# Kernel optimization log

Hardware: AMD Instinct MI355X
Metric: run time of the kernel (lower is better)

## Reference

```python
import jax, jax.numpy as jnp
import numpy as np

D_MODEL = 512
N_HEADS = 8
BLOCK = 512
D_HEAD = D_MODEL // N_HEADS
SCALE = D_HEAD ** -0.5


def _linear_params(key, d_in, d_out):
    kw, kb = jax.random.split(key)
    bound = 1.0 / np.sqrt(d_in)
    w = jax.random.uniform(kw, (d_in, d_out), jnp.float32, -bound, bound)
    b = jax.random.uniform(kb, (d_out,), jnp.float32, -bound, bound)
    return w, b


def setup_inputs() -> dict:
    key = jax.random.key(0)
    keys = jax.random.split(key, 10)
    x = jax.random.normal(keys[0], (4, 8192, D_MODEL), jnp.float32)
    names = ["lq", "lk", "lv", "lo", "gq", "gk", "gv", "go"]
    inp = {"x": x}
    for i, n in enumerate(names):
        w, b = _linear_params(keys[1 + i], D_MODEL, D_MODEL)
        inp[n + "_w"] = w
        inp[n + "_b"] = b
    gw, gb = _linear_params(keys[9], 2 * D_MODEL, D_MODEL)
    inp["gate_w"] = gw
    inp["gate_b"] = gb
    return inp


def _attend(q, k, v):
    # q,k,v: (..., L, H, Dh) -> (..., L, H, Dh)
    scores = jnp.einsum("...qhd,...khd->...hqk", q, k) * SCALE
    probs = jax.nn.softmax(scores, axis=-1)
    return jnp.einsum("...hqk,...khd->...qhd", probs, v)


def reference(x, lq_w, lq_b, lk_w, lk_b, lv_w, lv_b, lo_w, lo_b,
              gq_w, gq_b, gk_w, gk_b, gv_w, gv_b, go_w, go_b,
              gate_w, gate_b):
    B, S, D = x.shape
    nb = S // BLOCK
    xb = x.reshape(B, nb, BLOCK, D)

    def heads(t, L_axes):
        return t.reshape(t.shape[:-1] + (N_HEADS, D_HEAD))

    # block-local attention (all blocks batched)
    Q = heads(xb @ lq_w + lq_b, None)  # (B, nb, bs, H, Dh)
    K = heads(xb @ lk_w + lk_b, None)
    V = heads(xb @ lv_w + lv_b, None)
    loc = _attend(Q, K, V).reshape(B, nb, BLOCK, D)
    local_out = (loc @ lo_w + lo_b).reshape(B, S, D)

    # pooled block summaries: AdaptiveAvgPool1d(1) == mean over block length
    pooled = xb.mean(axis=2)  # (B, nb, D)
    Qg = heads(pooled @ gq_w + gq_b, None)  # (B, nb, H, Dh)
    Kg = heads(pooled @ gk_w + gk_b, None)
    Vg = heads(pooled @ gv_w + gv_b, None)
    glob = _attend(Qg, Kg, Vg).reshape(B, nb, D)
    glob = glob @ go_w + go_b  # (B, nb, D)

    # broadcast each block summary to its tokens
    global_out = jnp.repeat(glob, BLOCK, axis=1)  # (B, S, D)

    gate_in = jnp.concatenate([local_out, global_out], axis=-1)
    gate = jax.nn.sigmoid(gate_in @ gate_w + gate_b)
    return gate * local_out + (1.0 - gate) * global_out
```

## Files before the change

### kernel.cpp

```cpp
#include <hip/hip_runtime.h>
#include <math.h>

typedef unsigned short u16;
typedef short s16;
typedef u16 u16x8 __attribute__((ext_vector_type(8)));
typedef u16 u16x4 __attribute__((ext_vector_type(4)));
typedef s16 s16x8 __attribute__((ext_vector_type(8)));
typedef float f32x4 __attribute__((ext_vector_type(4)));
typedef unsigned u32x4 __attribute__((ext_vector_type(4)));

__device__ __forceinline__ float b2f(u16 u) { return __uint_as_float(((unsigned)u) << 16); }
__device__ __forceinline__ u16 f2b(float f) {
  unsigned x = __float_as_uint(f);
  unsigned r = x + 0x7fffu + ((x >> 16) & 1u);
  return (u16)(r >> 16);
}
__device__ __forceinline__ unsigned cvtpk(float a, float b) {
  unsigned r;
  asm("v_cvt_pk_bf16_f32 %0, %1, %2" : "=v"(r) : "v"(a), "v"(b));
  return r;
}
union PkH { u32x4 w; s16x8 h; };
union Pk2 { unsigned w[2]; u16x4 h; };

#define SCALE 0.125f
#define SCLG2E 0.1803368801111137f
#define DM 512
#define NTOK 32768

typedef __attribute__((address_space(1))) unsigned int as1_u32;
typedef __attribute__((address_space(3))) unsigned int as3_u32;
__device__ __forceinline__ void gl2lds16(const u16* g, u16* s) {
  __builtin_amdgcn_global_load_lds((as1_u32*)g, (as3_u32*)s, 16, 0, 0);
}

__global__ __launch_bounds__(256)
void conv_psum(const float* __restrict__ X, u16* __restrict__ Xb,
               float* __restrict__ Psum)
{
  __shared__ float ps[4][512];
  const int tid = threadIdx.x;
  const int c8 = (tid & 63) * 8;
  const int rg = tid >> 6;
  const size_t tok0 = (size_t)blockIdx.x * 64;
  f32x4 s0 = {0.f, 0.f, 0.f, 0.f}, s1 = {0.f, 0.f, 0.f, 0.f};
  for (int it = 0; it < 16; ++it) {
    const size_t tok = tok0 + it * 4 + rg;
    const float* xp = X + tok * DM + c8;
    f32x4 a = *(const f32x4*)xp;
    f32x4 b = *(const f32x4*)(xp + 4);
    Pk2 p0, p1;
    p0.w[0] = cvtpk(a[0], a[1]); p0.w[1] = cvtpk(a[2], a[3]);
    p1.w[0] = cvtpk(b[0], b[1]); p1.w[1] = cvtpk(b[2], b[3]);
    *(u16x4*)(Xb + tok * DM + c8)     = p0.h;
    *(u16x4*)(Xb + tok * DM + c8 + 4) = p1.h;
    s0 += a; s1 += b;
  }
  *(f32x4*)&ps[rg][c8]     = s0;
  *(f32x4*)&ps[rg][c8 + 4] = s1;
  __syncthreads();
#pragma unroll
  for (int i = 0; i < 2; ++i) {
    const int col = tid + i * 256;
    Psum[(size_t)blockIdx.x * DM + col] =
        ps[0][col] + ps[1][col] + ps[2][col] + ps[3][col];
  }
}

__global__ __launch_bounds__(256)
void pool_prep(const float* __restrict__ Psum, u16* __restrict__ PB)
{
  const int g = blockIdx.x, tid = threadIdx.x;
#pragma unroll
  for (int i = 0; i < 2; ++i) {
    const int col = tid + i * 256;
    float v = 0.f;
#pragma unroll
    for (int s = 0; s < 8; ++s) v += Psum[(size_t)(g * 8 + s) * DM + col];
    PB[(size_t)g * DM + col] = f2b(v * (1.f / 512.f));
  }
}

__global__ __launch_bounds__(256)
void trans_w(const float* w0, const float* w1, const float* w2, const float* w3,
             const float* w4, const float* w5, const float* w6, const float* w7,
             const float* w8, const float* w9, u16* __restrict__ WT)
{
  __shared__ float t[32][33];
  const int z = blockIdx.z;
  const float* W = (z == 0) ? w0 : (z == 1) ? w1 : (z == 2) ? w2 : (z == 3) ? w3 :
                   (z == 4) ? w4 : (z == 5) ? w5 : (z == 6) ? w6 : (z == 7) ? w7 :
                   (z == 8) ? w8 : w9;
  u16* D = WT + (size_t)z * DM * DM;
  const int tx = threadIdx.x & 31, ty = threadIdx.x >> 5;
  const int n0 = blockIdx.x * 32, k0 = blockIdx.y * 32;
#pragma unroll
  for (int j = 0; j < 4; ++j)
    t[ty + j * 8][tx] = W[(size_t)(k0 + ty + j * 8) * DM + n0 + tx];
  __syncthreads();
#pragma unroll
  for (int j = 0; j < 4; ++j)
    D[(size_t)(n0 + ty + j * 8) * DM + k0 + tx] = f2b(t[tx][ty + j * 8]);
}

__global__ __launch_bounds__(256)
void conv_w(const float* __restrict__ W, u16* __restrict__ D)
{
  const size_t i = ((size_t)blockIdx.x * 256 + threadIdx.x) * 8;
  f32x4 a = *(const f32x4*)(W + i);
  f32x4 b = *(const f32x4*)(W + i + 4);
  Pk2 p0, p1;
  p0.w[0] = cvtpk(a[0], a[1]); p0.w[1] = cvtpk(a[2], a[3]);
  p1.w[0] = cvtpk(b[0], b[1]); p1.w[1] = cvtpk(b[2], b[3]);
  *(u16x4*)(D + i)     = p0.h;
  *(u16x4*)(D + i + 4) = p1.h;
}

__global__ __launch_bounds__(256)
void bc_kernel(const float* __restrict__ go_b, const float* __restrict__ gate_w,
               const float* __restrict__ gate_b, float* __restrict__ bc)
{
  __shared__ float red[8][32];
  const int tid = threadIdx.x;
  const int jj = tid & 31, part = tid >> 5;
  const int j = blockIdx.x * 32 + jj;
  float p = 0.f;
#pragma unroll
  for (int i = 0; i < 64; ++i) {
    const int k = part * 64 + i;
    p = fmaf(go_b[k], gate_w[(size_t)(512 + k) * DM + j], p);
  }
  red[part][jj] = p;
  __syncthreads();
  if (tid < 32) {
    float v = gate_b[blockIdx.x * 32 + tid];
#pragma unroll
    for (int s = 0; s < 8; ++s) v += red[s][tid];
    bc[blockIdx.x * 32 + tid] = v;
  }
}

template<int EPI>
__global__ __launch_bounds__(256)
void gemm_mfma(const u16* __restrict__ A, const u16* __restrict__ Wt,
               const float* __restrict__ bias, u16* __restrict__ Cb,
               float* __restrict__ Cf, float outscale,
               const float* __restrict__ GG)
{
  __shared__ u16 As[2][128 * 64];
  __shared__ u16 Bs[2][128 * 64];
  const int tid = threadIdx.x;
  const int w = tid >> 6, l = tid & 63;
  const int l15 = l & 15, gl = l >> 4;
  const int wm = w >> 1, wn = w & 1;

  int mt, nt;
  if (gridDim.y == 256) {
    const int H = blockIdx.y * 4 + blockIdx.x;
    const int xcd = H & 7, i = H >> 3;
    mt = xcd * 32 + (i >> 2);
    nt = i & 3;
  } else {
    mt = blockIdx.y; nt = blockIdx.x;
  }
  const int m0 = mt * 128, n0 = nt * 128;

  const int srow = l >> 3;
  const int scol = ((l & 7) ^ (srow & 7)) * 8;
  const u16* Ag = A  + (size_t)(m0 + w * 32 + srow) * DM + scol;
  const u16* Bg = Wt + (size_t)(n0 + w * 32 + srow) * DM + scol;

  auto stage = [&](int t, int b) {
    const int k0 = t * 64;
#pragma unroll
    for (int c = 0; c < 4; ++c) {
      gl2lds16(Ag + (size_t)(c * 8) * DM + k0, &As[b][(w * 32 + c * 8) * 64]);
      gl2lds16(Bg + (size_t)(c * 8) * DM + k0, &Bs[b][(w * 32 + c * 8) * 64]);
    }
  };

  f32x4 acc[4][4];
#pragma unroll
  for (int i = 0; i < 4; ++i)
#pragma unroll
    for (int j = 0; j < 4; ++j) acc[i][j] = {0.f, 0.f, 0.f, 0.f};

  const int xorv = l15 & 7;
  stage(0, 0);
#pragma unroll
  for (int t = 0; t < 8; ++t) {
    if (t < 7) {
      stage(t + 1, (t + 1) & 1);
      asm volatile("s_waitcnt vmcnt(8)" ::: "memory");
    } else {
      asm volatile("s_waitcnt vmcnt(0)" ::: "memory");
    }
    __builtin_amdgcn_s_barrier();
    __builtin_amdgcn_sched_barrier(0);
    const int b = t & 1;
#pragma unroll
    for (int kd = 0; kd < 2; ++kd) {
      const int go = ((gl + 4 * kd) ^ xorv) * 8;
      s16x8 af[4], bfr[4];
#pragma unroll
      for (int f = 0; f < 4; ++f) {
        af[f]  = *(const s16x8*)&As[b][(wm * 64 + f * 16 + l15) * 64 + go];
        bfr[f] = *(const s16x8*)&Bs[b][(wn * 64 + f * 16 + l15) * 64 + go];
      }
#pragma unroll
      for (int fm = 0; fm < 4; ++fm)
#pragma unroll
        for (int fn = 0; fn < 4; ++fn) {
          if (EPI == 2)
            acc[fm][fn] = __builtin_amdgcn_mfma_f32_16x16x32_bf16(
                af[fm], bfr[fn], acc[fm][fn], 0, 0, 0);
          else
            acc[fm][fn] = __builtin_amdgcn_mfma_f32_16x16x32_bf16(
                bfr[fn], af[fm], acc[fm][fn], 0, 0, 0);
        }
    }
    __builtin_amdgcn_s_barrier();
  }

  if (EPI == 2) {
#pragma unroll
    for (int fn = 0; fn < 4; ++fn) {
      const int n = n0 + wn * 64 + fn * 16 + l15;
      const float bn = bias[n];
      const int d = n & 63, ghn = n >> 6;
#pragma unroll
      for (int fm = 0; fm < 4; ++fm) {
        const int m = m0 + wm * 64 + fm * 16 + gl * 4;
        const int f = (m & 63) >> 4;
        const int pos = ((f >> 1) << 5) | (gl << 3) | ((f & 1) << 2);
        Pk2 p;
        p.w[0] = cvtpk(acc[fm][fn][0] + bn, acc[fm][fn][1] + bn);
        p.w[1] = cvtpk(acc[fm][fn][2] + bn, acc[fm][fn][3] + bn);
        *(u16x4*)(Cb + ((size_t)(((m >> 9) * 8 + ghn) * 64 + d)) * 512
                     + ((m & 511) >> 6) * 64 + pos) = p.h;
      }
    }
  } else {
#pragma unroll
    for (int fm = 0; fm < 4; ++fm) {
      const int m = m0 + wm * 64 + fm * 16 + l15;
      const int brow = m >> 9;
#pragma unroll
      for (int fn = 0; fn < 4; ++fn) {
        const int nb = n0 + wn * 64 + fn * 16 + gl * 4;
        if (EPI == 0) {
          f32x4 b4 = *(const f32x4*)&bias[nb];
          f32x4 v = (acc[fm][fn] + b4) * outscale;
          Pk2 p;
          p.w[0] = cvtpk(v[0], v[1]);
          p.w[1] = cvtpk(v[2], v[3]);
          *(u16x4*)(Cb + (size_t)m * DM + nb) = p.h;
        } else if (EPI == 3) {
          Pk2 p;
          p.w[0] = cvtpk(acc[fm][fn][0], acc[fm][fn][1]);
          p.w[1] = cvtpk(acc[fm][fn][2], acc[fm][fn][3]);
          *(u16x4*)(Cb + (size_t)m * DM + nb) = p.h;
        } else {
          f32x4 z = acc[fm][fn] + *(const f32x4*)&GG[(size_t)brow * 1024 + 512 + nb];
          u16x4 lo4 = *(const u16x4*)(A + (size_t)m * DM + nb);
          f32x4 go4 = *(const f32x4*)&GG[(size_t)brow * 1024 + nb];
          f32x4 res;
#pragma unroll
          for (int r = 0; r < 4; ++r) {
            float g = 1.f / (1.f + __expf(-z[r]));
            res[r] = g * b2f(lo4[r]) + (1.f - g) * go4[r];
          }
          *(f32x4*)(Cf + (size_t)m * DM + nb) = res;
        }
      }
    }
  }
}

__global__ __launch_bounds__(256)
void gemm64(const u16* __restrict__ A,
            const u16* B0, const u16* B1, const u16* B2,
            const float* b0, const float* b1, const float* b2,
            float* __restrict__ Out, int ldo)
{
  __shared__ u16 As[2][64 * 64];
  __shared__ u16 Bs[2][128 * 64];
  const int tid = threadIdx.x;
  const int w = tid >> 6, l = tid & 63;
  const int l15 = l & 15, gl = l >> 4;
  const int bx = blockIdx.x;
  const int grp = bx >> 2;
  const u16* Bt = ((grp == 0) ? B0 : (grp == 1) ? B1 : B2)
                  + (size_t)(bx & 3) * 128 * DM;
  const float* bias = (grp == 0) ? b0 : (grp == 1) ? b1 : b2;

  const int srow = l >> 3;
  const int scol = ((l & 7) ^ (srow & 7)) * 8;
  const u16* Ag = A  + (size_t)(w * 16 + srow) * DM + scol;
  const u16* Bg = Bt + (size_t)(w * 32 + srow) * DM + scol;

  auto stage = [&](int t, int b) {
    const int k0 = t * 64;
#pragma unroll
    for (int c = 0; c < 2; ++c)
      gl2lds16(Ag + (size_t)(c * 8) * DM + k0, &As[b][(w * 16 + c * 8) * 64]);
#pragma unroll
    for (int c = 0; c < 4; ++c)
      gl2lds16(Bg + (size_t)(c * 8) * DM + k0, &Bs[b][(w * 32 + c * 8) * 64]);
  };

  f32x4 acc[4][2];
#pragma unroll
  for (int i = 0; i < 4; ++i)
#pragma unroll
    for (int j = 0; j < 2; ++j) acc[i][j] = {0.f, 0.f, 0.f, 0.f};

  const int xorv = l15 & 7;
  stage(0, 0);
#pragma unroll
  for (int t = 0; t < 8; ++t) {
    if (t < 7) {
      stage(t + 1, (t + 1) & 1);
      asm volatile("s_waitcnt vmcnt(6)" ::: "memory");
    } else {
      asm volatile("s_waitcnt vmcnt(0)" ::: "memory");
    }
    __builtin_amdgcn_s_barrier();
    __builtin_amdgcn_sched_barrier(0);
    const int b = t & 1;
#pragma unroll
    for (int kd = 0; kd < 2; ++kd) {
      const int go = ((gl + 4 * kd) ^ xorv) * 8;
      s16x8 af[4], bfr[2];
#pragma unroll
      for (int f = 0; f < 4; ++f)
        af[f] = *(const s16x8*)&As[b][(f * 16 + l15) * 64 + go];
#pragma unroll
      for (int f = 0; f < 2; ++f)
        bfr[f] = *(const s16x8*)&Bs[b][(w * 32 + f * 16 + l15) * 64 + go];
#pragma unroll
      for (int fm = 0; fm < 4; ++fm)
#pragma unroll
        for (int fn = 0; fn < 2; ++fn)
          acc[fm][fn] = __builtin_amdgcn_mfma_f32_16x16x32_bf16(
              bfr[fn], af[fm], acc[fm][fn], 0, 0, 0);
    }
    __builtin_amdgcn_s_barrier();
  }

#pragma unroll
  for (int fm = 0; fm < 4; ++fm) {
    const int m = fm * 16 + l15;
#pragma unroll
    for (int fn = 0; fn < 2; ++fn) {
      const int nloc = w * 32 + fn * 16 + gl * 4;
      f32x4 b4 = *(const f32x4*)&bias[(bx & 3) * 128 + nloc];
      *(f32x4*)&Out[(size_t)m * ldo + bx * 128 + nloc] = acc[fm][fn] + b4;
    }
  }
}

__global__ __launch_bounds__(512, 4)
void attn_mfma(const u16* __restrict__ Q, const u16* __restrict__ K,
               const u16* __restrict__ VT, u16* __restrict__ CTX)
{
  __shared__ u16 Ks[64 * 64];
  __shared__ u16 VsT[64 * 64];
  const int tid = threadIdx.x;
  const int w = tid >> 6, l = tid & 63;
  const int l15 = l & 15, gl = l >> 4;
  const int g = blockIdx.x, h = blockIdx.y, qh = blockIdx.z;
  const int t0 = g * 512;
  const int fb = h * 64;
  const int q0 = t0 + qh * 256 + w * 32;
  const u16* VTb = VT + ((size_t)(g * 8 + h) * 64) * 512;

  s16x8 qf[2][2];
#pragma unroll
  for (int fq = 0; fq < 2; ++fq)
#pragma unroll
    for (int kd = 0; kd < 2; ++kd)
      qf[fq][kd] = *(const s16x8*)(Q + (size_t)(q0 + fq * 16 + l15) * DM
                                     + fb + gl * 8 + kd * 32);

  f32x4 o[2][4];
#pragma unroll
  for (int i = 0; i < 2; ++i)
#pragma unroll
    for (int j = 0; j < 4; ++j) o[i][j] = {0.f, 0.f, 0.f, 0.f};
  f32x4 psv[2] = {{0.f,0.f,0.f,0.f}, {0.f,0.f,0.f,0.f}};

  const int srow = tid >> 3;
  const int swg = ((tid & 7) ^ ((tid >> 3) & 7)) * 8;
  const u16* Kg = K + (size_t)(t0 + srow) * DM + fb + swg;
  const u16* Vg = VTb + (size_t)srow * 512 + swg;
  s16x8 kreg = *(const s16x8*)Kg;
  s16x8 vreg = *(const s16x8*)Vg;
  const int sw = l15 & 7;

  for (int kc = 0; kc < 8; ++kc) {
    __syncthreads();
    *(s16x8*)&Ks[tid * 8]  = kreg;
    *(s16x8*)&VsT[tid * 8] = vreg;
    __syncthreads();
    if (kc < 7) {
      kreg = *(const s16x8*)(Kg + (size_t)(kc + 1) * 64 * DM);
      vreg = *(const s16x8*)(Vg + (kc + 1) * 64);
    }

    f32x4 s[4][2];
#pragma unroll
    for (int i = 0; i < 4; ++i)
#pragma unroll
      for (int j = 0; j < 2; ++j) s[i][j] = {0.f, 0.f, 0.f, 0.f};
#pragma unroll
    for (int kd = 0; kd < 2; ++kd) {
      s16x8 kf[4];
#pragma unroll
      for (int fm = 0; fm < 4; ++fm)
        kf[fm] = *(const s16x8*)&Ks[(fm * 16 + l15) * 64 + ((gl + 4 * kd) ^ sw) * 8];
#pragma unroll
      for (int fm = 0; fm < 4; ++fm)
#pragma unroll
        for (int fq = 0; fq < 2; ++fq)
          s[fm][fq] = __builtin_amdgcn_mfma_f32_16x16x32_bf16(
              kf[fm], qf[fq][kd], s[fm][fq], 0, 0, 0);
    }

#pragma unroll
    for (int fq = 0; fq < 2; ++fq)
#pragma unroll
      for (int fm = 0; fm < 4; ++fm) {
#pragma unroll
        for (int r = 0; r < 4; ++r) s[fm][fq][r] = exp2f(s[fm][fq][r]);
        psv[fq] += s[fm][fq];
      }

    PkH pf[2][2];
#pragma unroll
    for (int ka = 0; ka < 2; ++ka)
#pragma unroll
      for (int fq = 0; fq < 2; ++fq) {
        pf[ka][fq].w[0] = cvtpk(s[2 * ka][fq][0], s[2 * ka][fq][1]);
        pf[ka][fq].w[1] = cvtpk(s[2 * ka][fq][2], s[2 * ka][fq][3]);
        pf[ka][fq].w[2] = cvtpk(s[2 * ka + 1][fq][0], s[2 * ka + 1][fq][1]);
        pf[ka][fq].w[3] = cvtpk(s[2 * ka + 1][fq][2], s[2 * ka + 1][fq][3]);
      }

#pragma unroll
    for (int ka = 0; ka < 2; ++ka)
#pragma unroll
      for (int fd = 0; fd < 4; ++fd) {
        s16x8 vf = *(const s16x8*)&VsT[(fd * 16 + l15) * 64 + ((ka * 4 + gl) ^ sw) * 8];
#pragma unroll
        for (int qm = 0; qm < 2; ++qm)
          o[qm][fd] = __builtin_amdgcn_mfma_f32_16x16x32_bf16(
              pf[ka][qm].h, vf, o[qm][fd], 0, 0, 0);
      }
  }

  float l_[2];
#pragma unroll
  for (int fq = 0; fq < 2; ++fq) {
    float t = (psv[fq][0] + psv[fq][1]) + (psv[fq][2] + psv[fq][3]);
    t += __shfl_xor(t, 16);
    t += __shfl_xor(t, 32);
    l_[fq] = t;
  }
#pragma unroll
  for (int qm = 0; qm < 2; ++qm) {
    const float i0 = 1.f / __shfl(l_[qm], gl * 4 + 0);
    const float i1 = 1.f / __shfl(l_[qm], gl * 4 + 1);
    const float i2 = 1.f / __shfl(l_[qm], gl * 4 + 2);
    const float i3 = 1.f / __shfl(l_[qm], gl * 4 + 3);
#pragma unroll
    for (int fd = 0; fd < 4; ++fd) {
      const size_t base = (size_t)(q0 + qm * 16 + gl * 4) * DM + fb + fd * 16 + l15;
      CTX[base]          = f2b(o[qm][fd][0] * i0);
      CTX[base + DM]     = f2b(o[qm][fd][1] * i1);
      CTX[base + 2 * DM] = f2b(o[qm][fd][2] * i2);
      CTX[base + 3 * DM] = f2b(o[qm][fd][3] * i3);
    }
  }
}

__global__ __launch_bounds__(256)
void gattn(const float* __restrict__ QKVg, u16* __restrict__ GlB)
{
  __shared__ float q[16][64], k[16][64], v[16][64];
  __shared__ float sc[16][16];
  const int bh = blockIdx.x;
  const int b = bh >> 3, h = bh & 7;
  const int tid = threadIdx.x;
  for (int idx = tid; idx < 1024; idx += 256) {
    const int n = idx >> 6, d = idx & 63;
    const size_t off = (size_t)(b * 16 + n) * 1536 + h * 64 + d;
    q[n][d] = QKVg[off]; k[n][d] = QKVg[off + 512]; v[n][d] = QKVg[off + 1024];
  }
  __syncthreads();
  {
    const int qq = tid >> 4, kk = tid & 15;
    float s = 0.f;
#pragma unroll
    for (int d = 0; d < 64; ++d) s = fmaf(q[qq][d], k[kk][d], s);
    sc[qq][kk] = s * SCALE;
  }
  __syncthreads();
  if (tid < 16) {
    float mx = -INFINITY;
#pragma unroll
    for (int j = 0; j < 16; ++j) mx = fmaxf(mx, sc[tid][j]);
    float e[16]; float sum = 0.f;
#pragma unroll
    for (int j = 0; j < 16; ++j) { e[j] = __expf(sc[tid][j] - mx); sum += e[j]; }
    const float inv = 1.f / sum;
#pragma unroll
    for (int j = 0; j < 16; ++j) sc[tid][j] = e[j] * inv;
  }
  __syncthreads();
  for (int idx = tid; idx < 1024; idx += 256) {
    const int qq = idx >> 6, d = idx & 63;
    float o = 0.f;
#pragma unroll
    for (int j = 0; j < 16; ++j) o = fmaf(sc[qq][j], v[j][d], o);
    GlB[(size_t)(b * 16 + qq) * DM + h * 64 + d] = f2b(o);
  }
}

extern "C" void kernel_launch(void* const* d_in, const int* in_sizes, int n_in,
                              void* d_out, int out_size, void* d_ws, size_t ws_size,
                              hipStream_t stream)
{
  const float* x      = (const float*)d_in[0];
  const float* lq_w   = (const float*)d_in[1];
  const float* lq_b   = (const float*)d_in[2];
  const float* lk_w   = (const float*)d_in[3];
  const float* lk_b   = (const float*)d_in[4];
  const float* lv_w   = (const float*)d_in[5];
  const float* lv_b   = (const float*)d_in[6];
  const float* lo_w   = (const float*)d_in[7];
  const float* lo_b   = (const float*)d_in[8];
  const float* gq_w   = (const float*)d_in[9];
  const float* gq_b   = (const float*)d_in[10];
  const float* gk_w   = (const float*)d_in[11];
  const float* gk_b   = (const float*)d_in[12];
  const float* gv_w   = (const float*)d_in[13];
  const float* gv_b   = (const float*)d_in[14];
  const float* go_w   = (const float*)d_in[15];
  const float* go_b   = (const float*)d_in[16];
  const float* gate_w = (const float*)d_in[17];
  const float* gate_b = (const float*)d_in[18];
  float* out = (float*)d_out;

  const size_t NE = (size_t)NTOK * DM;
  const size_t DD = (size_t)DM * DM;
  char* ws = (char*)d_ws;
  u16* Qb  = (u16*)ws;
  u16* Kb  = Qb + NE;
  u16* VT  = Kb + NE;
  u16* WT  = VT + NE;
  u16* goD = WT + 10 * DD;
  u16* WcT = goD + DD;
  u16* PB  = WcT + DD;
  u16* GlB = PB + 64 * DM;
  float* scr  = (float*)(GlB + 64 * DM);
  float* Psum = scr;
  float* QKVg = Psum + 512 * DM;
  float* GG   = QKVg + (size_t)64 * 1536;
  float* bc   = GG + (size_t)64 * 1024;
  u16* xb = (u16*)d_out;
  u16* LOCAL = Kb;

  u16* WTq  = WT;
  u16* WTk  = WT + 1 * DD;
  u16* WTv  = WT + 2 * DD;
  u16* WTo  = WT + 3 * DD;
  u16* WTg  = WT + 4 * DD;
  u16* WTgq = WT + 5 * DD;
  u16* WTgk = WT + 6 * DD;
  u16* WTgv = WT + 7 * DD;
  u16* WTgo = WT + 8 * DD;
  u16* WTg2 = WT + 9 * DD;

  conv_psum<<<512, 256, 0, stream>>>(x, xb, Psum);
  trans_w<<<dim3(16, 16, 10), 256, 0, stream>>>(
      lq_w, lk_w, lv_w, lo_w, gate_w, gq_w, gk_w, gv_w, go_w,
      gate_w + DD, WT);
  conv_w<<<128, 256, 0, stream>>>(go_w, goD);
  bc_kernel<<<16, 256, 0, stream>>>(go_b, gate_w, gate_b, bc);
  pool_prep<<<64, 256, 0, stream>>>(Psum, PB);

  const dim3 gg(4, 256), bb(256);
  gemm_mfma<0><<<gg, bb, 0, stream>>>(xb, WTq, lq_b, Qb, nullptr, SCLG2E, nullptr);
  gemm_mfma<0><<<gg, bb, 0, stream>>>(xb, WTk, lk_b, Kb, nullptr, 1.0f, nullptr);
  gemm_mfma<2><<<gg, bb, 0, stream>>>(xb, WTv, lv_b, VT, nullptr, 1.0f, nullptr);
  gemm_mfma<3><<<dim3(4, 4), bb, 0, stream>>>(WTg2, goD, nullptr, WcT, nullptr, 1.0f, nullptr);

  attn_mfma<<<dim3(64, 8, 2), 512, 0, stream>>>(Qb, Kb, VT, Qb );
  gemm_mfma<0><<<gg, bb, 0, stream>>>(Qb , WTo, lo_b, LOCAL, nullptr, 1.0f, nullptr);

  gemm64<<<12, 256, 0, stream>>>(PB, WTgq, WTgk, WTgv, gq_b, gk_b, gv_b, QKVg, 1536);
  gattn<<<32, 256, 0, stream>>>(QKVg, GlB);
  gemm64<<<8, 256, 0, stream>>>(GlB, WTgo, WcT, WcT, go_b, bc, bc, GG, 1024);

  gemm_mfma<1><<<gg, bb, 0, stream>>>(LOCAL, WTg, nullptr, nullptr, out, 1.0f, GG);
}
```

Before: 243.1 us.

## Fuse Q/K/V projection GEMMs into one launch and compute softmax row sums via MFMA

Replaces three separate Q, K and V projection GEMM launches with one kernel over a 12x256 grid, where each tile picks its weight, bias and epilogue from its N-tile index. This cuts launch overhead and lets all three projections share one wave schedule with better occupancy. In the attention kernel, the per-lane exp-sum accumulation and cross-lane shuffle reduction are replaced by an extra MFMA against a vector of bf16 ones, so the normalisers come out in the accumulator layout. That sum now uses the bf16-rounded probabilities, matching the P·V numerator, at the cost of a few more MFMA issues.

```diff
diff --git a/kernel.cpp b/kernel.cpp
--- a/kernel.cpp
+++ b/kernel.cpp
@@ -140,6 +140,131 @@
   }
 }
 
+__global__ __launch_bounds__(256)
+void gemm_qkv(const u16* __restrict__ A,
+              const u16* __restrict__ WTq, const u16* __restrict__ WTk,
+              const u16* __restrict__ WTv,
+              const float* __restrict__ bq, const float* __restrict__ bk,
+              const float* __restrict__ bv,
+              u16* __restrict__ Qb, u16* __restrict__ Kb, u16* __restrict__ VT)
+{
+  __shared__ u16 As[2][128 * 64];
+  __shared__ u16 Bs[2][128 * 64];
+  const int tid = threadIdx.x;
+  const int w = tid >> 6, l = tid & 63;
+  const int l15 = l & 15, gl = l >> 4;
+  const int wm = w >> 1, wn = w & 1;
+
+  const int H = blockIdx.y * 12 + blockIdx.x;
+  const int xcd = H & 7, i = H >> 3;
+  const int mt = xcd * 32 + i / 12;
+  const int nt = i % 12;
+  const int sel = nt >> 2;
+  const int m0 = mt * 128;
+  const int n0 = (nt & 3) * 128;
+
+  const u16* Wt = (sel == 0) ? WTq : (sel == 1) ? WTk : WTv;
+  const float* bias = (sel == 0) ? bq : (sel == 1) ? bk : bv;
+
+  const int srow = l >> 3;
+  const int scol = ((l & 7) ^ (srow & 7)) * 8;
+  const u16* Ag = A  + (size_t)(m0 + w * 32 + srow) * DM + scol;
+  const u16* Bg = Wt + (size_t)(n0 + w * 32 + srow) * DM + scol;
+
+  auto stage = [&](int t, int b) {
+    const int k0 = t * 64;
+#pragma unroll
+    for (int c = 0; c < 4; ++c) {
+      gl2lds16(Ag + (size_t)(c * 8) * DM + k0, &As[b][(w * 32 + c * 8) * 64]);
+      gl2lds16(Bg + (size_t)(c * 8) * DM + k0, &Bs[b][(w * 32 + c * 8) * 64]);
+    }
+  };
+
+  f32x4 acc[4][4];
+#pragma unroll
+  for (int ii = 0; ii < 4; ++ii)
+#pragma unroll
+    for (int j = 0; j < 4; ++j) acc[ii][j] = {0.f, 0.f, 0.f, 0.f};
+
+  const int xorv = l15 & 7;
+  stage(0, 0);
+#pragma unroll
+  for (int t = 0; t < 8; ++t) {
+    if (t < 7) {
+      stage(t + 1, (t + 1) & 1);
+      asm volatile("s_waitcnt vmcnt(8)" ::: "memory");
+    } else {
+      asm volatile("s_waitcnt vmcnt(0)" ::: "memory");
+    }
+    __builtin_amdgcn_s_barrier();
+    __builtin_amdgcn_sched_barrier(0);
+    const int b = t & 1;
+#pragma unroll
+    for (int kd = 0; kd < 2; ++kd) {
+      const int go = ((gl + 4 * kd) ^ xorv) * 8;
+      s16x8 af[4], bfr[4];
+#pragma unroll
+      for (int f = 0; f < 4; ++f) {
+        af[f]  = *(const s16x8*)&As[b][(wm * 64 + f * 16 + l15) * 64 + go];
+        bfr[f] = *(const s16x8*)&Bs[b][(wn * 64 + f * 16 + l15) * 64 + go];
+      }
+      if (sel == 2) {
+#pragma unroll
+        for (int fm = 0; fm < 4; ++fm)
+#pragma unroll
+          for (int fn = 0; fn < 4; ++fn)
+            acc[fm][fn] = __builtin_amdgcn_mfma_f32_16x16x32_bf16(
+                af[fm], bfr[fn], acc[fm][fn], 0, 0, 0);
+      } else {
+#pragma unroll
+        for (int fm = 0; fm < 4; ++fm)
+#pragma unroll
+          for (int fn = 0; fn < 4; ++fn)
+            acc[fm][fn] = __builtin_amdgcn_mfma_f32_16x16x32_bf16(
+                bfr[fn], af[fm], acc[fm][fn], 0, 0, 0);
+      }
+    }
+    __builtin_amdgcn_s_barrier();
+  }
+
+  if (sel == 2) {
+#pragma unroll
+    for (int fn = 0; fn < 4; ++fn) {
+      const int n = n0 + wn * 64 + fn * 16 + l15;
+      const float bn = bias[n];
+      const int d = n & 63, ghn = n >> 6;
+#pragma unroll
+      for (int fm = 0; fm < 4; ++fm) {
+        const int m = m0 + wm * 64 + fm * 16 + gl * 4;
+        const int f = (m & 63) >> 4;
+        const int pos = ((f >> 1) << 5) | (gl << 3) | ((f & 1) << 2);
+        Pk2 p;
+        p.w[0] = cvtpk(acc[fm][fn][0] + bn, acc[fm][fn][1] + bn);
+        p.w[1] = cvtpk(acc[fm][fn][2] + bn, acc[fm][fn][3] + bn);
+        *(u16x4*)(VT + ((size_t)(((m >> 9) * 8 + ghn) * 64 + d)) * 512
+                     + ((m & 511) >> 6) * 64 + pos) = p.h;
+      }
+    }
+  } else {
+    u16* Cb = (sel == 0) ? Qb : Kb;
+    const float sc = (sel == 0) ? SCLG2E : 1.0f;
+#pragma unroll
+    for (int fm = 0; fm < 4; ++fm) {
+      const int m = m0 + wm * 64 + fm * 16 + l15;
+#pragma unroll
+      for (int fn = 0; fn < 4; ++fn) {
+        const int nb = n0 + wn * 64 + fn * 16 + gl * 4;
+        f32x4 b4 = *(const f32x4*)&bias[nb];
+        f32x4 v = (acc[fm][fn] + b4) * sc;
+        Pk2 p;
+        p.w[0] = cvtpk(v[0], v[1]);
+        p.w[1] = cvtpk(v[2], v[3]);
+        *(u16x4*)(Cb + (size_t)m * DM + nb) = p.h;
+      }
+    }
+  }
+}
+
 template<int EPI>
 __global__ __launch_bounds__(256)
 void gemm_mfma(const u16* __restrict__ A, const u16* __restrict__ Wt,
@@ -210,68 +335,43 @@
 #pragma unroll
       for (int fm = 0; fm < 4; ++fm)
 #pragma unroll
-        for (int fn = 0; fn < 4; ++fn) {
-          if (EPI == 2)
-            acc[fm][fn] = __builtin_amdgcn_mfma_f32_16x16x32_bf16(
-                af[fm], bfr[fn], acc[fm][fn], 0, 0, 0);
-          else
-            acc[fm][fn] = __builtin_amdgcn_mfma_f32_16x16x32_bf16(
-                bfr[fn], af[fm], acc[fm][fn], 0, 0, 0);
+        for (int fn = 0; fn < 4; ++fn)
+          acc[fm][fn] = __builtin_amdgcn_mfma_f32_16x16x32_bf16(
+              bfr[fn], af[fm], acc[fm][fn], 0, 0, 0);
+    }
+    __builtin_amdgcn_s_barrier();
+  }
+
+#pragma unroll
+  for (int fm = 0; fm < 4; ++fm) {
+    const int m = m0 + wm * 64 + fm * 16 + l15;
+    const int brow = m >> 9;
+#pragma unroll
+    for (int fn = 0; fn < 4; ++fn) {
+      const int nb = n0 + wn * 64 + fn * 16 + gl * 4;
+      if (EPI == 0) {
+        f32x4 b4 = *(const f32x4*)&bias[nb];
+        f32x4 v = (acc[fm][fn] + b4) * outscale;
+        Pk2 p;
+        p.w[0] = cvtpk(v[0], v[1]);
+        p.w[1] = cvtpk(v[2], v[3]);
+        *(u16x4*)(Cb + (size_t)m * DM + nb) = p.h;
+      } else if (EPI == 3) {
+        Pk2 p;
+        p.w[0] = cvtpk(acc[fm][fn][0], acc[fm][fn][1]);
+        p.w[1] = cvtpk(acc[fm][fn][2], acc[fm][fn][3]);
+        *(u16x4*)(Cb + (size_t)m * DM + nb) = p.h;
+      } else {
+        f32x4 z = acc[fm][fn] + *(const f32x4*)&GG[(size_t)brow * 1024 + 512 + nb];
+        u16x4 lo4 = *(const u16x4*)(A + (size_t)m * DM + nb);
+        f32x4 go4 = *(const f32x4*)&GG[(size_t)brow * 1024 + nb];
+        f32x4 res;
+#pragma unroll
+        for (int r = 0; r < 4; ++r) {
+          float g = 1.f / (1.f + __expf(-z[r]));
+          res[r] = g * b2f(lo4[r]) + (1.f - g) * go4[r];
         }
-    }
-    __builtin_amdgcn_s_barrier();
-  }
-
-  if (EPI == 2) {
-#pragma unroll
-    for (int fn = 0; fn < 4; ++fn) {
-      const int n = n0 + wn * 64 + fn * 16 + l15;
-      const float bn = bias[n];
-      const int d = n & 63, ghn = n >> 6;
-#pragma unroll
-      for (int fm = 0; fm < 4; ++fm) {
-        const int m = m0 + wm * 64 + fm * 16 + gl * 4;
-        const int f = (m & 63) >> 4;
-        const int pos = ((f >> 1) << 5) | (gl << 3) | ((f & 1) << 2);
-        Pk2 p;
-        p.w[0] = cvtpk(acc[fm][fn][0] + bn, acc[fm][fn][1] + bn);
-        p.w[1] = cvtpk(acc[fm][fn][2] + bn, acc[fm][fn][3] + bn);
-        *(u16x4*)(Cb + ((size_t)(((m >> 9) * 8 + ghn) * 64 + d)) * 512
-                     + ((m & 511) >> 6) * 64 + pos) = p.h;
-      }
-    }
-  } else {
-#pragma unroll
-    for (int fm = 0; fm < 4; ++fm) {
-      const int m = m0 + wm * 64 + fm * 16 + l15;
-      const int brow = m >> 9;
-#pragma unroll
-      for (int fn = 0; fn < 4; ++fn) {
-        const int nb = n0 + wn * 64 + fn * 16 + gl * 4;
-        if (EPI == 0) {
-          f32x4 b4 = *(const f32x4*)&bias[nb];
-          f32x4 v = (acc[fm][fn] + b4) * outscale;
-          Pk2 p;
-          p.w[0] = cvtpk(v[0], v[1]);
-          p.w[1] = cvtpk(v[2], v[3]);
-          *(u16x4*)(Cb + (size_t)m * DM + nb) = p.h;
-        } else if (EPI == 3) {
-          Pk2 p;
-          p.w[0] = cvtpk(acc[fm][fn][0], acc[fm][fn][1]);
-          p.w[1] = cvtpk(acc[fm][fn][2], acc[fm][fn][3]);
-          *(u16x4*)(Cb + (size_t)m * DM + nb) = p.h;
-        } else {
-          f32x4 z = acc[fm][fn] + *(const f32x4*)&GG[(size_t)brow * 1024 + 512 + nb];
-          u16x4 lo4 = *(const u16x4*)(A + (size_t)m * DM + nb);
-          f32x4 go4 = *(const f32x4*)&GG[(size_t)brow * 1024 + nb];
-          f32x4 res;
-#pragma unroll
-          for (int r = 0; r < 4; ++r) {
-            float g = 1.f / (1.f + __expf(-z[r]));
-            res[r] = g * b2f(lo4[r]) + (1.f - g) * go4[r];
-          }
-          *(f32x4*)(Cf + (size_t)m * DM + nb) = res;
-        }
+        *(f32x4*)(Cf + (size_t)m * DM + nb) = res;
       }
     }
   }
@@ -383,12 +483,16 @@
       qf[fq][kd] = *(const s16x8*)(Q + (size_t)(q0 + fq * 16 + l15) * DM
                                      + fb + gl * 8 + kd * 32);
 
+  s16x8 vones;
+#pragma unroll
+  for (int j = 0; j < 8; ++j) vones[j] = (s16)0x3F80;
+
   f32x4 o[2][4];
 #pragma unroll
   for (int i = 0; i < 2; ++i)
 #pragma unroll
     for (int j = 0; j < 4; ++j) o[i][j] = {0.f, 0.f, 0.f, 0.f};
-  f32x4 psv[2] = {{0.f,0.f,0.f,0.f}, {0.f,0.f,0.f,0.f}};
+  f32x4 o_sum[2] = {{0.f,0.f,0.f,0.f}, {0.f,0.f,0.f,0.f}};
 
   const int srow = tid >> 3;
   const int swg = ((tid & 7) ^ ((tid >> 3) & 7)) * 8;
@@ -430,11 +534,9 @@
 #pragma unroll
     for (int fq = 0; fq < 2; ++fq)
 #pragma unroll
-      for (int fm = 0; fm < 4; ++fm) {
+      for (int fm = 0; fm < 4; ++fm)
 #pragma unroll
         for (int r = 0; r < 4; ++r) s[fm][fq][r] = exp2f(s[fm][fq][r]);
-        psv[fq] += s[fm][fq];
-      }
 
     PkH pf[2][2];
 #pragma unroll
@@ -448,7 +550,7 @@
       }
 
 #pragma unroll
-    for (int ka = 0; ka < 2; ++ka)
+    for (int ka = 0; ka < 2; ++ka) {
 #pragma unroll
       for (int fd = 0; fd < 4; ++fd) {
         s16x8 vf = *(const s16x8*)&VsT[(fd * 16 + l15) * 64 + ((ka * 4 + gl) ^ sw) * 8];
@@ -457,29 +559,25 @@
           o[qm][fd] = __builtin_amdgcn_mfma_f32_16x16x32_bf16(
               pf[ka][qm].h, vf, o[qm][fd], 0, 0, 0);
       }
-  }
-
-  float l_[2];
-#pragma unroll
-  for (int fq = 0; fq < 2; ++fq) {
-    float t = (psv[fq][0] + psv[fq][1]) + (psv[fq][2] + psv[fq][3]);
-    t += __shfl_xor(t, 16);
-    t += __shfl_xor(t, 32);
-    l_[fq] = t;
-  }
+#pragma unroll
+      for (int qm = 0; qm < 2; ++qm)
+        o_sum[qm] = __builtin_amdgcn_mfma_f32_16x16x32_bf16(
+            pf[ka][qm].h, vones, o_sum[qm], 0, 0, 0);
+    }
+  }
+
 #pragma unroll
   for (int qm = 0; qm < 2; ++qm) {
-    const float i0 = 1.f / __shfl(l_[qm], gl * 4 + 0);
-    const float i1 = 1.f / __shfl(l_[qm], gl * 4 + 1);
-    const float i2 = 1.f / __shfl(l_[qm], gl * 4 + 2);
-    const float i3 = 1.f / __shfl(l_[qm], gl * 4 + 3);
+    f32x4 inv4;
+#pragma unroll
+    for (int r = 0; r < 4; ++r) inv4[r] = 1.f / o_sum[qm][r];
 #pragma unroll
     for (int fd = 0; fd < 4; ++fd) {
       const size_t base = (size_t)(q0 + qm * 16 + gl * 4) * DM + fb + fd * 16 + l15;
-      CTX[base]          = f2b(o[qm][fd][0] * i0);
-      CTX[base + DM]     = f2b(o[qm][fd][1] * i1);
-      CTX[base + 2 * DM] = f2b(o[qm][fd][2] * i2);
-      CTX[base + 3 * DM] = f2b(o[qm][fd][3] * i3);
+      CTX[base]          = f2b(o[qm][fd][0] * inv4[0]);
+      CTX[base + DM]     = f2b(o[qm][fd][1] * inv4[1]);
+      CTX[base + 2 * DM] = f2b(o[qm][fd][2] * inv4[2]);
+      CTX[base + 3 * DM] = f2b(o[qm][fd][3] * inv4[3]);
     }
   }
 }
@@ -591,9 +689,8 @@
   pool_prep<<<64, 256, 0, stream>>>(Psum, PB);
 
   const dim3 gg(4, 256), bb(256);
-  gemm_mfma<0><<<gg, bb, 0, stream>>>(xb, WTq, lq_b, Qb, nullptr, SCLG2E, nullptr);
-  gemm_mfma<0><<<gg, bb, 0, stream>>>(xb, WTk, lk_b, Kb, nullptr, 1.0f, nullptr);
-  gemm_mfma<2><<<gg, bb, 0, stream>>>(xb, WTv, lv_b, VT, nullptr, 1.0f, nullptr);
+  gemm_qkv<<<dim3(12, 256), bb, 0, stream>>>(xb, WTq, WTk, WTv,
+                                             lq_b, lk_b, lv_b, Qb, Kb, VT);
   gemm_mfma<3><<<dim3(4, 4), bb, 0, stream>>>(WTg2, goD, nullptr, WcT, nullptr, 1.0f, nullptr);
 
   attn_mfma<<<dim3(64, 8, 2), 512, 0, stream>>>(Qb, Kb, VT, Qb );
```

After: 284.4 us. +17.0%, slower.
